# Kernel tuning notes

Hardware: AMD Instinct MI355X
Metric: run time of the kernel (lower is better)

## Reference

```python
import jax, jax.numpy as jnp
import numpy as np

HIDDEN_DIM = 2048
N = 4  # expansion_rate
LAYER_IDX = 0
S_ALPHA = 0.01
S_BETA = 0.01
EPS = 1e-5


def setup_inputs() -> dict:
    key = jax.random.key(0)
    k1, k2, k3, k4, k5 = jax.random.split(key, 5)
    batch, seq = 4, 2048
    layer_output = jax.random.normal(k1, (batch, seq, HIDDEN_DIM), dtype=jnp.float32)
    hidden_states = jax.random.normal(k2, (batch, seq, N, HIDDEN_DIM), dtype=jnp.float32)
    # static base matrices (initialization from the torch module)
    B = jnp.ones((1, N), dtype=jnp.float32)
    Am = jnp.zeros((N, 1), dtype=jnp.float32).at[LAYER_IDX % N, 0].set(1.0)
    Ar = jnp.eye(N, dtype=jnp.float32)
    # dynamic parameters
    s_alpha = jnp.full((N, N), S_ALPHA, dtype=jnp.float32)
    s_beta = jnp.full((1, N), S_BETA, dtype=jnp.float32)
    W_beta = jax.random.normal(k3, (HIDDEN_DIM, N), dtype=jnp.float32) * 0.02
    W_m = jax.random.normal(k4, (HIDDEN_DIM, N), dtype=jnp.float32) * 0.02
    W_r = jax.random.normal(k5, (HIDDEN_DIM, N, N), dtype=jnp.float32) * 0.02
    return {
        "layer_output": layer_output,
        "hidden_states": hidden_states,
        "B": B,
        "Am": Am,
        "Ar": Ar,
        "s_alpha": s_alpha,
        "s_beta": s_beta,
        "W_beta": W_beta,
        "W_m": W_m,
        "W_r": W_r,
    }


def reference(layer_output, hidden_states, B, Am, Ar, s_alpha, s_beta, W_beta, W_m, W_r):
    # hidden_states: [b, s, n, d]; layer_output: [b, s, d]
    # --- dynamic matrices ---
    mu = jnp.mean(hidden_states, axis=-1, keepdims=True)
    var = jnp.var(hidden_states, axis=-1, keepdims=True)
    H_norm = (hidden_states - mu) * jax.lax.rsqrt(var + EPS)  # layer_norm, no affine
    H_bar = H_norm.mean(axis=2)  # [b, s, d]

    delta_B = jnp.tanh(H_bar @ W_beta)            # [b, s, n]
    B_dyn = s_beta[0] * delta_B + B[0]            # [b, s, n]
    delta_Am = jnp.tanh(H_bar @ W_m)              # [b, s, n]
    Am_dyn = s_alpha[:, 0] * delta_Am + Am[:, 0]  # [b, s, n]
    delta_Ar = jnp.tanh(jnp.einsum('bsd,dij->bsij', H_bar, W_r))  # [b, s, n, n]
    Ar_dyn = s_alpha * delta_Ar + Ar              # [b, s, n, n]

    # --- combine ---
    depth = B_dyn[..., None] * layer_output[:, :, None, :]                       # [b,s,n,d]
    mixed = jnp.einsum('bsn,bsnd->bsd', Am_dyn, hidden_states)[:, :, None, :]    # [b,s,1,d] broadcasts over n
    residual = jnp.einsum('bsij,bsjd->bsid', Ar_dyn, hidden_states)              # [b,s,n,d]
    return depth + mixed + residual
```

## Files before the change

### kernel.cpp

```cpp
#include <hip/hip_runtime.h>
#include <hip/hip_fp16.h>

#define D     2048
#define BLK   512
#define EPSV  1e-5f

typedef _Float16 h2 __attribute__((ext_vector_type(2)));

__device__ __forceinline__ unsigned int pkh(float a, float b) {
    return __builtin_bit_cast(unsigned int, __builtin_amdgcn_cvt_pkrtz(a, b));
}
__device__ __forceinline__ h2 ash2(unsigned int u) {
    return __builtin_bit_cast(h2, u);
}

__global__ __launch_bounds__(256) void wt_kernel(
    const float* __restrict__ Wb, const float* __restrict__ Wm,
    const float* __restrict__ Wr, unsigned int* __restrict__ Wq,
    float* __restrict__ S)
{
    const int c = blockIdx.x;
    const int t = threadIdx.x;
    const float* src;
    int stride;
    if (c < 4)       { src = Wb + c;       stride = 4;  }
    else if (c < 8)  { src = Wm + (c - 4); stride = 4;  }
    else             { src = Wr + (c - 8); stride = 16; }

    float s = 0.f;
    #pragma unroll
    for (int k = 0; k < 4; ++k) {
        int p = t + 256 * k;
        float a = src[(2 * p)     * stride];
        float b = src[(2 * p + 1) * stride];
        s += a + b;
        Wq[c * 1024 + p] = pkh(a, b);
    }
    __shared__ float rsum[4];
    #pragma unroll
    for (int off = 32; off; off >>= 1) s += __shfl_xor(s, off, 64);
    if ((t & 63) == 0) rsum[t >> 6] = s;
    __syncthreads();
    if (t == 0) S[c] = rsum[0] + rsum[1] + rsum[2] + rsum[3];
}

__global__ __launch_bounds__(BLK) void hc_kernel(
    const float* __restrict__ lo,
    const float* __restrict__ hs,
    const float* __restrict__ Bm,
    const float* __restrict__ Am,
    const float* __restrict__ Ar,
    const float* __restrict__ s_alpha,
    const float* __restrict__ s_beta,
    const unsigned int* __restrict__ Wq,
    const float* __restrict__ S,
    float* __restrict__ out)
{
    __shared__ unsigned int hq[4][1024];
    __shared__ float Rl[24][4];
    __shared__ float sred[8][2];
    __shared__ float coefs[24];

    const int tid  = threadIdx.x;
    const int wave = tid >> 6;
    const int lane = tid & 63;
    const int row  = wave >> 1;
    const int half = wave & 1;
    const long tok = blockIdx.x;

    const float4* hs4  = (const float4*)(hs + tok * (long)(4 * D));
    const float4* lo4  = (const float4*)(lo + tok * (long)D);
    float4*       out4 = (float4*)(out + tok * (long)(4 * D));

    float4 hv[4];
    const int base = row * 512 + half * 256 + lane;
    #pragma unroll
    for (int k = 0; k < 4; ++k) hv[k] = hs4[base + 64 * k];
    float4 lv = lo4[tid];

    float s = 0.f, q = 0.f;
    uint2* hq2w = (uint2*)hq[row];
    #pragma unroll
    for (int k = 0; k < 4; ++k) {
        float4 v = hv[k];
        s += v.x + v.y + v.z + v.w;
        q += v.x * v.x + v.y * v.y + v.z * v.z + v.w * v.w;
        uint2 p;
        p.x = pkh(v.x, v.y);
        p.y = pkh(v.z, v.w);
        hq2w[half * 256 + 64 * k + lane] = p;
    }
    #pragma unroll
    for (int off = 32; off; off >>= 1) {
        s += __shfl_xor(s, off, 64);
        q += __shfl_xor(q, off, 64);
    }
    if (lane == 0) { sred[wave][0] = s; sred[wave][1] = q; }
    __syncthreads();

    float acc[3][4];
    #pragma unroll
    for (int j = 0; j < 3; ++j)
        #pragma unroll
        for (int n = 0; n < 4; ++n) acc[j][n] = 0.f;

    const int c0 = wave * 3;
    const uint2* Wq2 = (const uint2*)Wq;

    #pragma unroll
    for (int k = 0; k < 8; ++k) {
        int i = 64 * k + lane;
        uint2 hr[4];
        #pragma unroll
        for (int n = 0; n < 4; ++n) hr[n] = ((const uint2*)hq[n])[i];
        uint2 wv[3];
        #pragma unroll
        for (int j = 0; j < 3; ++j) wv[j] = Wq2[(c0 + j) * 512 + i];
        #pragma unroll
        for (int j = 0; j < 3; ++j)
            #pragma unroll
            for (int n = 0; n < 4; ++n) {
                acc[j][n] = __builtin_amdgcn_fdot2(ash2(hr[n].x), ash2(wv[j].x), acc[j][n], false);
                acc[j][n] = __builtin_amdgcn_fdot2(ash2(hr[n].y), ash2(wv[j].y), acc[j][n], false);
            }
    }
    #pragma unroll
    for (int j = 0; j < 3; ++j)
        #pragma unroll
        for (int n = 0; n < 4; ++n) {
            #pragma unroll
            for (int off = 32; off; off >>= 1)
                acc[j][n] += __shfl_xor(acc[j][n], off, 64);
        }
    if (lane == 0) {
        #pragma unroll
        for (int j = 0; j < 3; ++j)
            #pragma unroll
            for (int n = 0; n < 4; ++n) Rl[c0 + j][n] = acc[j][n];
    }
    __syncthreads();

    if (tid < 24) {
        int c = tid;
        float Sc = S[c];
        float raw = 0.f;
        #pragma unroll
        for (int n = 0; n < 4; ++n) {
            float ss = sred[2 * n][0] + sred[2 * n + 1][0];
            float qq = sred[2 * n][1] + sred[2 * n + 1][1];
            float m   = ss * (1.f / D);
            float var = qq * (1.f / D) - m * m;
            float r   = rsqrtf(var + EPSV);
            raw += r * (Rl[c][n] - m * Sc);
        }
        raw *= 0.25f;
        float t = tanhf(raw);
        float cv;
        if (c < 4) {
            cv = s_beta[c] * t + Bm[c];
        } else if (c < 8) {
            int n = c - 4;
            cv = s_alpha[n * 4] * t + Am[n];
        } else {
            int ij = c - 8;
            cv = s_alpha[ij] * t + Ar[ij];
        }
        coefs[c] = cv;
    }
    __syncthreads();

    float Bd[4], Amd[4], Ard[4][4];
    #pragma unroll
    for (int n = 0; n < 4; ++n) { Bd[n] = coefs[n]; Amd[n] = coefs[4 + n]; }
    #pragma unroll
    for (int i = 0; i < 4; ++i)
        #pragma unroll
        for (int j = 0; j < 4; ++j) Ard[i][j] = coefs[8 + i * 4 + j];

    float4 h[4];
    #pragma unroll
    for (int n = 0; n < 4; ++n) {
        uint2 r = ((const uint2*)hq[n])[tid];
        h2 a = ash2(r.x), b = ash2(r.y);
        h[n].x = (float)a[0]; h[n].y = (float)a[1];
        h[n].z = (float)b[0]; h[n].w = (float)b[1];
    }
    float4 mx = {0.f, 0.f, 0.f, 0.f};
    #pragma unroll
    for (int n = 0; n < 4; ++n) {
        mx.x += Amd[n] * h[n].x; mx.y += Amd[n] * h[n].y;
        mx.z += Amd[n] * h[n].z; mx.w += Amd[n] * h[n].w;
    }
    #pragma unroll
    for (int i = 0; i < 4; ++i) {
        float4 o;
        o.x = Bd[i] * lv.x + mx.x;
        o.y = Bd[i] * lv.y + mx.y;
        o.z = Bd[i] * lv.z + mx.z;
        o.w = Bd[i] * lv.w + mx.w;
        #pragma unroll
        for (int j = 0; j < 4; ++j) {
            o.x += Ard[i][j] * h[j].x;
            o.y += Ard[i][j] * h[j].y;
            o.z += Ard[i][j] * h[j].z;
            o.w += Ard[i][j] * h[j].w;
        }
        out4[i * 512 + tid] = o;
    }
}

extern "C" void kernel_launch(void* const* d_in, const int* in_sizes, int n_in,
                              void* d_out, int out_size, void* d_ws, size_t ws_size,
                              hipStream_t stream) {
    const float* lo      = (const float*)d_in[0];
    const float* hs      = (const float*)d_in[1];
    const float* Bm      = (const float*)d_in[2];
    const float* Am      = (const float*)d_in[3];
    const float* Ar      = (const float*)d_in[4];
    const float* s_alpha = (const float*)d_in[5];
    const float* s_beta  = (const float*)d_in[6];
    const float* Wb      = (const float*)d_in[7];
    const float* Wm      = (const float*)d_in[8];
    const float* Wr      = (const float*)d_in[9];
    float* out = (float*)d_out;

    unsigned int* Wq = (unsigned int*)d_ws;
    float* S         = (float*)((char*)d_ws + 24 * 1024 * 4);

    wt_kernel<<<24, 256, 0, stream>>>(Wb, Wm, Wr, Wq, S);

    const int tokens = in_sizes[0] / D;
    hc_kernel<<<tokens, BLK, 0, stream>>>(lo, hs, Bm, Am, Ar, s_alpha, s_beta,
                                          Wq, S, out);
}
```

Measured before the change: 146.8 us.

## Use DPP wave reductions and retile projection GEMV with wider loads

Replaces the shuffle-based wavefront reductions with two cross-row shuffles followed by DPP row-shift adds, so the result ends up in lane 15. The projection dot products are retiled so each wave handles 6 coefficient columns by 2 hidden-state rows with 128-bit loads, instead of 3 columns by all 4 rows with 64-bit loads. This halves the loop trip count and cuts per-wave LDS traffic. In exchange, each weight element is now read by twice as many waves, and there are slightly more reductions per wave.

```diff
diff --git a/kernel.cpp b/kernel.cpp
--- a/kernel.cpp
+++ b/kernel.cpp
@@ -12,6 +12,21 @@
 }
 __device__ __forceinline__ h2 ash2(unsigned int u) {
     return __builtin_bit_cast(h2, u);
+}
+
+template<int CTRL>
+__device__ __forceinline__ float dppadd(float x) {
+    int y = __builtin_amdgcn_update_dpp(0, __builtin_bit_cast(int, x), CTRL, 0xf, 0xf, false);
+    return x + __builtin_bit_cast(float, y);
+}
+__device__ __forceinline__ float wave_sum(float x) {
+    x += __shfl_xor(x, 32, 64);
+    x += __shfl_xor(x, 16, 64);
+    x = dppadd<0x111>(x);
+    x = dppadd<0x112>(x);
+    x = dppadd<0x114>(x);
+    x = dppadd<0x118>(x);
+    return x;
 }
 
 __global__ __launch_bounds__(256) void wt_kernel(
@@ -56,7 +71,7 @@
     const float* __restrict__ S,
     float* __restrict__ out)
 {
-    __shared__ unsigned int hq[4][1024];
+    __shared__ __align__(16) unsigned int hq[4][1024];
     __shared__ float Rl[24][4];
     __shared__ float sred[8][2];
     __shared__ float coefs[24];
@@ -90,53 +105,44 @@
         p.y = pkh(v.z, v.w);
         hq2w[half * 256 + 64 * k + lane] = p;
     }
-    #pragma unroll
-    for (int off = 32; off; off >>= 1) {
-        s += __shfl_xor(s, off, 64);
-        q += __shfl_xor(q, off, 64);
-    }
-    if (lane == 0) { sred[wave][0] = s; sred[wave][1] = q; }
-    __syncthreads();
-
-    float acc[3][4];
-    #pragma unroll
-    for (int j = 0; j < 3; ++j)
-        #pragma unroll
-        for (int n = 0; n < 4; ++n) acc[j][n] = 0.f;
-
-    const int c0 = wave * 3;
-    const uint2* Wq2 = (const uint2*)Wq;
-
-    #pragma unroll
-    for (int k = 0; k < 8; ++k) {
+    s = wave_sum(s);
+    q = wave_sum(q);
+    if (lane == 15) { sred[wave][0] = s; sred[wave][1] = q; }
+    __syncthreads();
+
+    float acc[6][2];
+    #pragma unroll
+    for (int j = 0; j < 6; ++j) { acc[j][0] = 0.f; acc[j][1] = 0.f; }
+
+    const int c0 = (wave >> 1) * 6;
+    const int r0 = (wave & 1) * 2;
+    const uint4* Wq4 = (const uint4*)Wq;
+
+    #pragma unroll
+    for (int k = 0; k < 4; ++k) {
         int i = 64 * k + lane;
-        uint2 hr[4];
-        #pragma unroll
-        for (int n = 0; n < 4; ++n) hr[n] = ((const uint2*)hq[n])[i];
-        uint2 wv[3];
-        #pragma unroll
-        for (int j = 0; j < 3; ++j) wv[j] = Wq2[(c0 + j) * 512 + i];
-        #pragma unroll
-        for (int j = 0; j < 3; ++j)
-            #pragma unroll
-            for (int n = 0; n < 4; ++n) {
-                acc[j][n] = __builtin_amdgcn_fdot2(ash2(hr[n].x), ash2(wv[j].x), acc[j][n], false);
-                acc[j][n] = __builtin_amdgcn_fdot2(ash2(hr[n].y), ash2(wv[j].y), acc[j][n], false);
-            }
-    }
-    #pragma unroll
-    for (int j = 0; j < 3; ++j)
-        #pragma unroll
-        for (int n = 0; n < 4; ++n) {
-            #pragma unroll
-            for (int off = 32; off; off >>= 1)
-                acc[j][n] += __shfl_xor(acc[j][n], off, 64);
-        }
-    if (lane == 0) {
-        #pragma unroll
-        for (int j = 0; j < 3; ++j)
-            #pragma unroll
-            for (int n = 0; n < 4; ++n) Rl[c0 + j][n] = acc[j][n];
+        uint4 hA = ((const uint4*)hq[r0])[i];
+        uint4 hB = ((const uint4*)hq[r0 + 1])[i];
+        #pragma unroll
+        for (int j = 0; j < 6; ++j) {
+            uint4 w = Wq4[(c0 + j) * 256 + i];
+            acc[j][0] = __builtin_amdgcn_fdot2(ash2(hA.x), ash2(w.x), acc[j][0], false);
+            acc[j][0] = __builtin_amdgcn_fdot2(ash2(hA.y), ash2(w.y), acc[j][0], false);
+            acc[j][0] = __builtin_amdgcn_fdot2(ash2(hA.z), ash2(w.z), acc[j][0], false);
+            acc[j][0] = __builtin_amdgcn_fdot2(ash2(hA.w), ash2(w.w), acc[j][0], false);
+            acc[j][1] = __builtin_amdgcn_fdot2(ash2(hB.x), ash2(w.x), acc[j][1], false);
+            acc[j][1] = __builtin_amdgcn_fdot2(ash2(hB.y), ash2(w.y), acc[j][1], false);
+            acc[j][1] = __builtin_amdgcn_fdot2(ash2(hB.z), ash2(w.z), acc[j][1], false);
+            acc[j][1] = __builtin_amdgcn_fdot2(ash2(hB.w), ash2(w.w), acc[j][1], false);
+        }
+    }
+    #pragma unroll
+    for (int j = 0; j < 6; ++j) {
+        #pragma unroll
+        for (int r = 0; r < 2; ++r) {
+            float v = wave_sum(acc[j][r]);
+            if (lane == 15) Rl[c0 + j][r0 + r] = v;
+        }
     }
     __syncthreads();
 
```

Measured after the change: 207.9 us. 41.6% more time.

## Process eight tokens per block with register double-buffered prefetch of next token

Applied to the files above, without the earlier changes.

Each block now handles eight consecutive tokens in a loop instead of one, and issues the global loads for the next token's hidden states and layer output right after the first barrier, so they overlap the dot-product and output phases of the current token. This is meant to hide global load latency and amortize block launch overhead. It holds roughly twice as many hidden-state registers, which may lower occupancy. The grid shrinks to 1024 blocks, and the launch assumes the token count is divisible by eight.

```diff
diff --git a/kernel.cpp b/kernel.cpp
--- a/kernel.cpp
+++ b/kernel.cpp
@@ -3,6 +3,7 @@
 
 #define D     2048
 #define BLK   512
+#define TPB   8
 #define EPSV  1e-5f
 
 typedef _Float16 h2 __attribute__((ext_vector_type(2)));
@@ -56,7 +57,7 @@
     const float* __restrict__ S,
     float* __restrict__ out)
 {
-    __shared__ unsigned int hq[4][1024];
+    __shared__ __align__(16) unsigned int hq[4][1024];
     __shared__ float Rl[24][4];
     __shared__ float sred[8][2];
     __shared__ float coefs[24];
@@ -66,146 +67,166 @@
     const int lane = tid & 63;
     const int row  = wave >> 1;
     const int half = wave & 1;
-    const long tok = blockIdx.x;
-
-    const float4* hs4  = (const float4*)(hs + tok * (long)(4 * D));
-    const float4* lo4  = (const float4*)(lo + tok * (long)D);
-    float4*       out4 = (float4*)(out + tok * (long)(4 * D));
-
-    float4 hv[4];
-    const int base = row * 512 + half * 256 + lane;
-    #pragma unroll
-    for (int k = 0; k < 4; ++k) hv[k] = hs4[base + 64 * k];
-    float4 lv = lo4[tid];
-
-    float s = 0.f, q = 0.f;
-    uint2* hq2w = (uint2*)hq[row];
-    #pragma unroll
-    for (int k = 0; k < 4; ++k) {
-        float4 v = hv[k];
-        s += v.x + v.y + v.z + v.w;
-        q += v.x * v.x + v.y * v.y + v.z * v.z + v.w * v.w;
-        uint2 p;
-        p.x = pkh(v.x, v.y);
-        p.y = pkh(v.z, v.w);
-        hq2w[half * 256 + 64 * k + lane] = p;
+    const long tok0 = (long)blockIdx.x * TPB;
+    const int  base = row * 512 + half * 256 + lane;
+
+    float4 hva[4], hvb[4], lva, lvb;
+
+    {
+        const float4* hs4 = (const float4*)(hs + tok0 * (long)(4 * D));
+        const float4* lo4 = (const float4*)(lo + tok0 * (long)D);
+        #pragma unroll
+        for (int k = 0; k < 4; ++k) hva[k] = hs4[base + 64 * k];
+        lva = lo4[tid];
     }
-    #pragma unroll
-    for (int off = 32; off; off >>= 1) {
-        s += __shfl_xor(s, off, 64);
-        q += __shfl_xor(q, off, 64);
-    }
-    if (lane == 0) { sred[wave][0] = s; sred[wave][1] = q; }
-    __syncthreads();
-
-    float acc[3][4];
-    #pragma unroll
-    for (int j = 0; j < 3; ++j)
-        #pragma unroll
-        for (int n = 0; n < 4; ++n) acc[j][n] = 0.f;
-
-    const int c0 = wave * 3;
-    const uint2* Wq2 = (const uint2*)Wq;
-
-    #pragma unroll
-    for (int k = 0; k < 8; ++k) {
-        int i = 64 * k + lane;
-        uint2 hr[4];
-        #pragma unroll
-        for (int n = 0; n < 4; ++n) hr[n] = ((const uint2*)hq[n])[i];
-        uint2 wv[3];
-        #pragma unroll
-        for (int j = 0; j < 3; ++j) wv[j] = Wq2[(c0 + j) * 512 + i];
+
+    auto body = [&](float4 (&cur)[4], float4& curl,
+                    float4 (&nxt)[4], float4& nxtl,
+                    long tok, bool pf) {
+        float s = 0.f, q = 0.f;
+        uint2* hq2w = (uint2*)hq[row];
+        #pragma unroll
+        for (int k = 0; k < 4; ++k) {
+            float4 v = cur[k];
+            s += v.x + v.y + v.z + v.w;
+            q += v.x * v.x + v.y * v.y + v.z * v.z + v.w * v.w;
+            uint2 p;
+            p.x = pkh(v.x, v.y);
+            p.y = pkh(v.z, v.w);
+            hq2w[half * 256 + 64 * k + lane] = p;
+        }
+        #pragma unroll
+        for (int off = 32; off; off >>= 1) {
+            s += __shfl_xor(s, off, 64);
+            q += __shfl_xor(q, off, 64);
+        }
+        if (lane == 0) { sred[wave][0] = s; sred[wave][1] = q; }
+        __syncthreads();
+
+        if (pf) {
+            const float4* hs4n = (const float4*)(hs + (tok + 1) * (long)(4 * D));
+            const float4* lo4n = (const float4*)(lo + (tok + 1) * (long)D);
+            #pragma unroll
+            for (int k = 0; k < 4; ++k) nxt[k] = hs4n[base + 64 * k];
+            nxtl = lo4n[tid];
+        }
+
+        float acc[3][4];
         #pragma unroll
         for (int j = 0; j < 3; ++j)
             #pragma unroll
+            for (int n = 0; n < 4; ++n) acc[j][n] = 0.f;
+
+        const int c0 = wave * 3;
+        const uint2* Wq2 = (const uint2*)Wq;
+
+        #pragma unroll
+        for (int k = 0; k < 8; ++k) {
+            int i = 64 * k + lane;
+            uint2 hr[4];
+            #pragma unroll
+            for (int n = 0; n < 4; ++n) hr[n] = ((const uint2*)hq[n])[i];
+            uint2 wv[3];
+            #pragma unroll
+            for (int j = 0; j < 3; ++j) wv[j] = Wq2[(c0 + j) * 512 + i];
+            #pragma unroll
+            for (int j = 0; j < 3; ++j)
+                #pragma unroll
+                for (int n = 0; n < 4; ++n) {
+                    acc[j][n] = __builtin_amdgcn_fdot2(ash2(hr[n].x), ash2(wv[j].x), acc[j][n], false);
+                    acc[j][n] = __builtin_amdgcn_fdot2(ash2(hr[n].y), ash2(wv[j].y), acc[j][n], false);
+                }
+        }
+        #pragma unroll
+        for (int j = 0; j < 3; ++j)
+            #pragma unroll
             for (int n = 0; n < 4; ++n) {
-                acc[j][n] = __builtin_amdgcn_fdot2(ash2(hr[n].x), ash2(wv[j].x), acc[j][n], false);
-                acc[j][n] = __builtin_amdgcn_fdot2(ash2(hr[n].y), ash2(wv[j].y), acc[j][n], false);
-            }
-    }
-    #pragma unroll
-    for (int j = 0; j < 3; ++j)
+                #pragma unroll
+                for (int off = 32; off; off >>= 1)
+                    acc[j][n] += __shfl_xor(acc[j][n], off, 64);
+            }
+        if (lane == 0) {
+            #pragma unroll
+            for (int j = 0; j < 3; ++j)
+                #pragma unroll
+                for (int n = 0; n < 4; ++n) Rl[c0 + j][n] = acc[j][n];
+        }
+        __syncthreads();
+
+        if (tid < 24) {
+            int c = tid;
+            float Sc = S[c];
+            float raw = 0.f;
+            #pragma unroll
+            for (int n = 0; n < 4; ++n) {
+                float ss = sred[2 * n][0] + sred[2 * n + 1][0];
+                float qq = sred[2 * n][1] + sred[2 * n + 1][1];
+                float m   = ss * (1.f / D);
+                float var = qq * (1.f / D) - m * m;
+                float r   = rsqrtf(var + EPSV);
+                raw += r * (Rl[c][n] - m * Sc);
+            }
+            raw *= 0.25f;
+            float t = tanhf(raw);
+            float cv;
+            if (c < 4) {
+                cv = s_beta[c] * t + Bm[c];
+            } else if (c < 8) {
+                int n = c - 4;
+                cv = s_alpha[n * 4] * t + Am[n];
+            } else {
+                int ij = c - 8;
+                cv = s_alpha[ij] * t + Ar[ij];
+            }
+            coefs[c] = cv;
+        }
+        __syncthreads();
+
+        float Bd[4], Amd[4], Ard[4][4];
+        #pragma unroll
+        for (int n = 0; n < 4; ++n) { Bd[n] = coefs[n]; Amd[n] = coefs[4 + n]; }
+        #pragma unroll
+        for (int i = 0; i < 4; ++i)
+            #pragma unroll
+            for (int j = 0; j < 4; ++j) Ard[i][j] = coefs[8 + i * 4 + j];
+
+        float4 h[4];
         #pragma unroll
         for (int n = 0; n < 4; ++n) {
-            #pragma unroll
-            for (int off = 32; off; off >>= 1)
-                acc[j][n] += __shfl_xor(acc[j][n], off, 64);
-        }
-    if (lane == 0) {
-        #pragma unroll
-        for (int j = 0; j < 3; ++j)
-            #pragma unroll
-            for (int n = 0; n < 4; ++n) Rl[c0 + j][n] = acc[j][n];
-    }
-    __syncthreads();
-
-    if (tid < 24) {
-        int c = tid;
-        float Sc = S[c];
-        float raw = 0.f;
+            uint2 r = ((const uint2*)hq[n])[tid];
+            h2 a = ash2(r.x), b = ash2(r.y);
+            h[n].x = (float)a[0]; h[n].y = (float)a[1];
+            h[n].z = (float)b[0]; h[n].w = (float)b[1];
+        }
+        float4* out4 = (float4*)(out + tok * (long)(4 * D));
+        float4 mx = {0.f, 0.f, 0.f, 0.f};
         #pragma unroll
         for (int n = 0; n < 4; ++n) {
-            float ss = sred[2 * n][0] + sred[2 * n + 1][0];
-            float qq = sred[2 * n][1] + sred[2 * n + 1][1];
-            float m   = ss * (1.f / D);
-            float var = qq * (1.f / D) - m * m;
-            float r   = rsqrtf(var + EPSV);
-            raw += r * (Rl[c][n] - m * Sc);
-        }
-        raw *= 0.25f;
-        float t = tanhf(raw);
-        float cv;
-        if (c < 4) {
-            cv = s_beta[c] * t + Bm[c];
-        } else if (c < 8) {
-            int n = c - 4;
-            cv = s_alpha[n * 4] * t + Am[n];
-        } else {
-            int ij = c - 8;
-            cv = s_alpha[ij] * t + Ar[ij];
-        }
-        coefs[c] = cv;
-    }
-    __syncthreads();
-
-    float Bd[4], Amd[4], Ard[4][4];
-    #pragma unroll
-    for (int n = 0; n < 4; ++n) { Bd[n] = coefs[n]; Amd[n] = coefs[4 + n]; }
-    #pragma unroll
-    for (int i = 0; i < 4; ++i)
-        #pragma unroll
-        for (int j = 0; j < 4; ++j) Ard[i][j] = coefs[8 + i * 4 + j];
-
-    float4 h[4];
-    #pragma unroll
-    for (int n = 0; n < 4; ++n) {
-        uint2 r = ((const uint2*)hq[n])[tid];
-        h2 a = ash2(r.x), b = ash2(r.y);
-        h[n].x = (float)a[0]; h[n].y = (float)a[1];
-        h[n].z = (float)b[0]; h[n].w = (float)b[1];
-    }
-    float4 mx = {0.f, 0.f, 0.f, 0.f};
-    #pragma unroll
-    for (int n = 0; n < 4; ++n) {
-        mx.x += Amd[n] * h[n].x; mx.y += Amd[n] * h[n].y;
-        mx.z += Amd[n] * h[n].z; mx.w += Amd[n] * h[n].w;
-    }
-    #pragma unroll
-    for (int i = 0; i < 4; ++i) {
-        float4 o;
-        o.x = Bd[i] * lv.x + mx.x;
-        o.y = Bd[i] * lv.y + mx.y;
-        o.z = Bd[i] * lv.z + mx.z;
-        o.w = Bd[i] * lv.w + mx.w;
-        #pragma unroll
-        for (int j = 0; j < 4; ++j) {
-            o.x += Ard[i][j] * h[j].x;
-            o.y += Ard[i][j] * h[j].y;
-            o.z += Ard[i][j] * h[j].z;
-            o.w += Ard[i][j] * h[j].w;
-        }
-        out4[i * 512 + tid] = o;
+            mx.x += Amd[n] * h[n].x; mx.y += Amd[n] * h[n].y;
+            mx.z += Amd[n] * h[n].z; mx.w += Amd[n] * h[n].w;
+        }
+        #pragma unroll
+        for (int i = 0; i < 4; ++i) {
+            float4 o;
+            o.x = Bd[i] * curl.x + mx.x;
+            o.y = Bd[i] * curl.y + mx.y;
+            o.z = Bd[i] * curl.z + mx.z;
+            o.w = Bd[i] * curl.w + mx.w;
+            #pragma unroll
+            for (int j = 0; j < 4; ++j) {
+                o.x += Ard[i][j] * h[j].x;
+                o.y += Ard[i][j] * h[j].y;
+                o.z += Ard[i][j] * h[j].z;
+                o.w += Ard[i][j] * h[j].w;
+            }
+            out4[i * 512 + tid] = o;
+        }
+        __syncthreads();
+    };
+
+    for (int it = 0; it < TPB; it += 2) {
+        body(hva, lva, hvb, lvb, tok0 + it,     true);
+        body(hvb, lvb, hva, lva, tok0 + it + 1, it + 2 < TPB);
     }
 }
 
@@ -230,6 +251,6 @@
     wt_kernel<<<24, 256, 0, stream>>>(Wb, Wm, Wr, Wq, S);
 
     const int tokens = in_sizes[0] / D;
-    hc_kernel<<<tokens, BLK, 0, stream>>>(lo, hs, Bm, Am, Ar, s_alpha, s_beta,
-                                          Wq, S, out);
-}
+    hc_kernel<<<tokens / TPB, BLK, 0, stream>>>(lo, hs, Bm, Am, Ar, s_alpha, s_beta,
+                                                Wq, S, out);
+}
```

After: 152.7 us. +4.0%, slower.
